# Performance work log

Measured on AMD Instinct MI355X. Metric: run time of the kernel, lower is better.

The kernel has to match this reference:

```python
import jax, jax.numpy as jnp
import numpy as np

N = 50000      # nodes
E = 800000     # edges
IN = 128       # input feature dim
HID = 64       # out_channels per head
HEADS = 2
OUT = 40       # num classes
SLOPE = 0.2    # leaky relu negative slope
EPS = 1e-16    # PyG softmax denominator epsilon


def _xavier(key, shape):
    fan_out, fan_in = shape[0], shape[1]
    a = float(np.sqrt(6.0 / (fan_in + fan_out)))
    return jax.random.uniform(key, shape, minval=-a, maxval=a, dtype=jnp.float32)


def setup_inputs() -> dict:
    key = jax.random.key(0)
    ks = jax.random.split(key, 16)
    x = jax.random.normal(ks[0], (N, IN), dtype=jnp.float32)
    edge_index = jax.random.randint(ks[1], (2, E), 0, N, dtype=jnp.int64)
    # GAT layer 1: lin_l == lin_r (shared), weight [H*C, in], att [C, H]
    W1 = _xavier(ks[2], (HEADS * HID, IN))
    b1 = jnp.zeros((HEADS * HID,), jnp.float32)
    al1 = _xavier(ks[3], (HID, HEADS))
    ar1 = _xavier(ks[4], (HID, HEADS))
    # GAT layer 2: input dim = heads*hidden
    W2 = _xavier(ks[5], (HEADS * HID, HEADS * HID))
    b2 = jnp.zeros((HEADS * HID,), jnp.float32)
    al2 = _xavier(ks[6], (HID, HEADS))
    ar2 = _xavier(ks[7], (HID, HEADS))
    # post_mp: Linear(heads*hid, hid) -> Linear(hid, out)
    Wp1 = _xavier(ks[8], (HID, HEADS * HID))
    bp1 = jnp.zeros((HID,), jnp.float32)
    Wp2 = _xavier(ks[9], (OUT, HID))
    bp2 = jnp.zeros((OUT,), jnp.float32)
    return dict(x=x, edge_index=edge_index, W1=W1, b1=b1, al1=al1, ar1=ar1,
                W2=W2, b2=b2, al2=al2, ar2=ar2, Wp1=Wp1, bp1=bp1, Wp2=Wp2, bp2=bp2)


def gat_layer(x, edge_index, W, b, att_l, att_r):
    """One GAT layer: shared linear, per-edge leaky-relu scores,
    segment-softmax keyed by destination node, scatter-sum."""
    n = x.shape[0]
    xt = (x @ W.T + b).reshape(n, HEADS, HID)          # [N, H, C] (x_l == x_r)
    alpha_l = jnp.einsum('nhc,ch->nh', xt, att_l)      # [N, H]
    alpha_r = jnp.einsum('nhc,ch->nh', xt, att_r)      # [N, H]
    src, dst = edge_index[0], edge_index[1]            # j = source, i = dest
    e = jax.nn.leaky_relu(alpha_r[dst] + alpha_l[src], SLOPE)   # [E, H]
    # segment softmax over edges grouped by destination node
    seg_max = jax.ops.segment_max(e, dst, num_segments=n)       # [N, H]
    ex = jnp.exp(e - seg_max[dst])
    denom = jax.ops.segment_sum(ex, dst, num_segments=n)        # [N, H]
    alpha = ex / (denom[dst] + EPS)                              # [E, H]
    msg = alpha[:, :, None] * xt[src]                            # [E, H, C]
    out = jax.ops.segment_sum(msg, dst, num_segments=n)          # [N, H, C]
    return out.reshape(n, HEADS * HID)


def reference(x, edge_index, W1, b1, al1, ar1, W2, b2, al2, ar2, Wp1, bp1, Wp2, bp2):
    h = jax.nn.relu(gat_layer(x, edge_index, W1, b1, al1, ar1))
    h = jax.nn.relu(gat_layer(h, edge_index, W2, b2, al2, ar2))
    h = h @ Wp1.T + bp1
    h = h @ Wp2.T + bp2
    return jax.nn.log_softmax(h, axis=1)
```

## Files before the change

kernel.cpp:

```cpp
#include <hip/hip_runtime.h>
#include <hip/hip_fp16.h>
#include <cmath>

#define N_NODES 50000
#define N_EDGES 800000
#define F 128
#define OUT_DIM 40
#define SLOPE 0.2f
#define EPS_DEN 1e-16f

#define BK_SHIFT 7
#define BKSZ 128
#define NBK ((N_NODES + BKSZ - 1) / BKSZ)
#define BK_CAP2 2560
#define SC_CHUNK 2500
#define SC_BLOCKS ((N_EDGES + SC_CHUNK - 1) / SC_CHUNK)
#define GEMM_TILES ((N_NODES + 127) / 128)
#define A_BLOCKS (SC_BLOCKS + 25 + GEMM_TILES)
#define SMEM_BYTES 21504
#define POISON ((int)0xAAAAAAAA)

typedef _Float16 half8 __attribute__((ext_vector_type(8)));
typedef float floatx4 __attribute__((ext_vector_type(4)));

struct ScatterS { int sd[SC_CHUNK]; short sb[SC_CHUNK]; int h[NBK]; int lofs[NBK]; };
struct GemmS    { __half Ah[128][40]; __half Bh[128][40]; };
static_assert(sizeof(ScatterS) <= SMEM_BYTES, "scatter LDS");
static_assert(sizeof(GemmS)    <= SMEM_BYTES, "gemm LDS");

__device__ __forceinline__ int swz(int row, int chunk) {
  return row * 128 + ((chunk ^ (row & 15)) << 3);
}

__device__ inline float4 load4(const float* p) { return *(const float4*)p; }
__device__ inline float4 load4(const __half* p) {
  uint2 u = *(const uint2*)p;
  float2 a = __half22float2(*(__half2*)&u.x);
  float2 b = __half22float2(*(__half2*)&u.y);
  return make_float4(a.x, a.y, b.x, b.y);
}

__device__ __forceinline__ void scatter_phase(const int* __restrict__ ei,
    int* __restrict__ bcur, int* __restrict__ pairs, int it, int tid, char* smem_) {
  ScatterS* S = (ScatterS*)smem_;
  for (int i = tid; i < NBK; i += 256) S->h[i] = 0;
  __syncthreads();
  int base = it * SC_CHUNK;
  int end = base + SC_CHUNK; if (end > N_EDGES) end = N_EDGES;
  int cnt = end - base;
  for (int e = base + tid; e < end; e += 256) {
    int s = ei[e];
    int d = ei[N_EDGES + e];
    int b = d >> BK_SHIFT;
    S->sd[e - base] = (s << BK_SHIFT) | (d & (BKSZ - 1));
    S->sb[e - base] = (short)b;
    atomicAdd(&S->h[b], 1);
  }
  __syncthreads();
  for (int i = tid; i < NBK; i += 256)
    if (S->h[i]) {
      S->lofs[i] = i * BK_CAP2 + (atomicAdd(&bcur[i], S->h[i]) - POISON);
      S->h[i] = 0;
    }
  __syncthreads();
  for (int i = tid; i < cnt; i += 256) {
    int b = S->sb[i];
    int pos = S->lofs[b] + atomicAdd(&S->h[b], 1);
    pairs[pos] = S->sd[i];
  }
}

__device__ __forceinline__ void combine_phase(const float* __restrict__ Wp1,
    const float* __restrict__ bp1, const float* __restrict__ Wp2,
    const float* __restrict__ bp2, __half* __restrict__ Wch,
    float* __restrict__ bc, int it, int tid) {
  if (it < 24) {
    int idx = it * 256 + tid;
    int o = idx >> 7, k = idx & 127;
    float s = 0.f;
    if (o < OUT_DIM) {
#pragma unroll 8
      for (int j = 0; j < 64; ++j) s += Wp2[o * 64 + j] * Wp1[j * 128 + k];
    }
    Wch[o * 128 + k] = __float2half(s);
  } else if (tid < 48) {
    int o = tid;
    if (o < OUT_DIM) {
      float s = bp2[o];
      for (int j = 0; j < 64; ++j) s += Wp2[o * 64 + j] * bp1[j];
      bc[o] = s;
    } else {
      bc[o] = -1e30f;
    }
  }
}

__global__ void local_sort_fwd();
template <typename T>
__device__ __forceinline__ void gemm_phase(const T* __restrict__ A,
    const float* __restrict__ W, const float* __restrict__ b,
    const float* __restrict__ attl, const float* __restrict__ attr,
    __half* __restrict__ Ch, float* __restrict__ al, float* __restrict__ ar,
    int nrows, int tile, int tid, char* smem_) {
  GemmS* S = (GemmS*)smem_;
  int lane = tid & 63, wid = tid >> 6;
  int quad = lane >> 4, col = lane & 15;
  int r0 = tile * 128;
  int rowhalf = wid >> 1, colhalf = wid & 1;
  floatx4 acc[4][4] = {};
  for (int kc = 0; kc < 128; kc += 32) {
    for (int i = tid; i < 512; i += 256) {
      int row = i >> 2, seg = i & 3;
      int gr = r0 + row;
      float4 v0, v1;
      if (gr < nrows) {
        const T* p = A + (size_t)gr * 128 + kc + seg * 8;
        v0 = load4(p); v1 = load4(p + 4);
      } else { v0 = make_float4(0.f,0.f,0.f,0.f); v1 = v0; }
      __half2 h0 = __floats2half2_rn(v0.x, v0.y), h1 = __floats2half2_rn(v0.z, v0.w);
      __half2 h2 = __floats2half2_rn(v1.x, v1.y), h3 = __floats2half2_rn(v1.z, v1.w);
      uint4 pk; pk.x = *(unsigned*)&h0; pk.y = *(unsigned*)&h1;
      pk.z = *(unsigned*)&h2; pk.w = *(unsigned*)&h3;
      *(uint4*)&S->Ah[row][seg * 8] = pk;
      const float* q = W + (size_t)row * 128 + kc + seg * 8;
      float4 w0 = *(const float4*)q, w1 = *(const float4*)(q + 4);
      __half2 g0 = __floats2half2_rn(w0.x, w0.y), g1 = __floats2half2_rn(w0.z, w0.w);
      __half2 g2 = __floats2half2_rn(w1.x, w1.y), g3 = __floats2half2_rn(w1.z, w1.w);
      uint4 qk; qk.x = *(unsigned*)&g0; qk.y = *(unsigned*)&g1;
      qk.z = *(unsigned*)&g2; qk.w = *(unsigned*)&g3;
      *(uint4*)&S->Bh[row][seg * 8] = qk;
    }
    __syncthreads();
    half8 afr[4], bfr[4];
#pragma unroll
    for (int rt = 0; rt < 4; ++rt)
      afr[rt] = *(const half8*)&S->Ah[rowhalf * 64 + rt * 16 + col][quad * 8];
#pragma unroll
    for (int ct = 0; ct < 4; ++ct)
      bfr[ct] = *(const half8*)&S->Bh[colhalf * 64 + ct * 16 + col][quad * 8];
#pragma unroll
    for (int rt = 0; rt < 4; ++rt)
#pragma unroll
      for (int ct = 0; ct < 4; ++ct)
        acc[rt][ct] = __builtin_amdgcn_mfma_f32_16x16x32_f16(afr[rt], bfr[ct],
                                                             acc[rt][ct], 0, 0, 0);
    __syncthreads();
  }
  int head = colhalf;
  float bj[4], wl4[4], wr4[4];
#pragma unroll
  for (int ct = 0; ct < 4; ++ct) {
    int c = ct * 16 + col;
    bj[ct] = b[head * 64 + c];
    wl4[ct] = attl[c * 2 + head];
    wr4[ct] = attr[c * 2 + head];
  }
#pragma unroll
  for (int rt = 0; rt < 4; ++rt) {
#pragma unroll
    for (int reg = 0; reg < 4; ++reg) {
      int gr = r0 + rowhalf * 64 + rt * 16 + quad * 4 + reg;
      bool ok = gr < nrows;
      float pl = 0.f, pr = 0.f;
#pragma unroll
      for (int ct = 0; ct < 4; ++ct) {
        float v = acc[rt][ct][reg] + bj[ct];
        pl += v * wl4[ct]; pr += v * wr4[ct];
        if (ok) Ch[(size_t)gr * F + head * 64 + ct * 16 + col] = __float2half(v);
      }
      pl += __shfl_xor(pl, 1, 64); pr += __shfl_xor(pr, 1, 64);
      pl += __shfl_xor(pl, 2, 64); pr += __shfl_xor(pr, 2, 64);
      pl += __shfl_xor(pl, 4, 64); pr += __shfl_xor(pr, 4, 64);
      pl += __shfl_xor(pl, 8, 64); pr += __shfl_xor(pr, 8, 64);
      if (ok && col == 0) { al[gr * 2 + head] = pl; ar[gr * 2 + head] = pr; }
    }
  }
}

__global__ __launch_bounds__(256) void kernelA(const int* __restrict__ ei,
    int* __restrict__ bcur, int* __restrict__ pairs,
    const float* __restrict__ Wp1, const float* __restrict__ bp1,
    const float* __restrict__ Wp2, const float* __restrict__ bp2,
    __half* __restrict__ Wch, float* __restrict__ bc,
    const float* __restrict__ x, const float* __restrict__ W1,
    const float* __restrict__ b1, const float* __restrict__ al1,
    const float* __restrict__ ar1, __half* __restrict__ xh,
    float* __restrict__ al, float* __restrict__ ar) {
  __shared__ __align__(16) char smem[SMEM_BYTES];
  int bid = blockIdx.x, tid = threadIdx.x;
  if (bid < SC_BLOCKS) {
    scatter_phase(ei, bcur, pairs, bid, tid, smem);
  } else if (bid < SC_BLOCKS + 25) {
    combine_phase(Wp1, bp1, Wp2, bp2, Wch, bc, bid - SC_BLOCKS, tid);
  } else {
    gemm_phase<float>(x, W1, b1, al1, ar1, xh, al, ar, N_NODES,
                      bid - SC_BLOCKS - 25, tid, smem);
  }
}

__global__ __launch_bounds__(256) void local_sort(const int* __restrict__ bcur,
    const int* __restrict__ pairs, int* __restrict__ rowstart,
    int* __restrict__ rowend, int* __restrict__ srcs) {
  __shared__ int buf[BK_CAP2];
  __shared__ int sorted[BK_CAP2];
  __shared__ int hist[BKSZ];
  __shared__ int cur[BKSZ];
  int tid = threadIdx.x;
  int b = blockIdx.x;
  int base = b * BK_CAP2;
  int cnt = bcur[b] - POISON;
  if (cnt > BK_CAP2) cnt = BK_CAP2;
  if (cnt < 0) cnt = 0;
  if (tid < BKSZ) hist[tid] = 0;
  __syncthreads();
  for (int i = tid; i < cnt; i += 256) {
    int p = pairs[base + i];
    buf[i] = p;
    atomicAdd(&hist[p & (BKSZ - 1)], 1);
  }
  __syncthreads();
  if (tid < 64) {
    int lane = tid;
    int carry = 0;
#pragma unroll
    for (int c = 0; c < BKSZ; c += 64) {
      int v = hist[c + lane];
      int x = v;
#pragma unroll
      for (int off = 1; off < 64; off <<= 1) {
        int t = __shfl_up(x, off, 64);
        if (lane >= off) x += t;
      }
      int excl = carry + x - v;
      cur[c + lane] = excl;
      int node = b * BKSZ + c + lane;
      if (node < N_NODES) {
        rowstart[node] = base + excl;
        rowend[node]   = base + excl + v;
      }
      carry += __shfl(x, 63, 64);
    }
  }
  __syncthreads();
  for (int i = tid; i < cnt; i += 256) {
    int p = buf[i];
    int pos = atomicAdd(&cur[p & (BKSZ - 1)], 1);
    sorted[pos] = p >> BK_SHIFT;
  }
  __syncthreads();
  for (int i = tid; i < cnt; i += 256)
    srcs[base + i] = sorted[i];
}

__device__ __forceinline__ void agg_node_to_lds(const int* __restrict__ rowstart,
    const int* __restrict__ rowend, const int* __restrict__ srcs,
    const float* __restrict__ al, const float* __restrict__ ar,
    const __half* __restrict__ xsrc, __half* __restrict__ ldsA,
    float (*ebufw)[64], int* sbufw, int node, int ldsrow, int lane) {
  int g = lane >> 4, q = lane & 15;
  int head = q >> 3;
  if (node >= N_NODES) {
    if (g == 0) {
      uint4 z = {0, 0, 0, 0};
      *(uint4*)&ldsA[swz(ldsrow, q)] = z;
    }
    __builtin_amdgcn_wave_barrier();
    return;
  }
  int start = rowstart[node], end = rowend[node];
  float2 arv = *(const float2*)(ar + (size_t)node * 2);
  float ar0 = arv.x, ar1 = arv.y;
  const float* wrow = &ebufw[head][0];
  const __half* xbase = xsrc + q * 8;
  float acc[8] = {};
  float dl0 = 0.f, dl1 = 0.f;
  for (int c = start; c < end; c += 64) {
    int j = c + lane;
    float e0 = 0.f, e1 = 0.f; int soff = 0;
    if (j < end) {
      int s = srcs[j];
      soff = s << BK_SHIFT;
      float2 a = *(const float2*)(al + (size_t)s * 2);
      float s0 = a.x + ar0; s0 = (s0 > 0.f) ? s0 : SLOPE * s0;
      float s1 = a.y + ar1; s1 = (s1 > 0.f) ? s1 : SLOPE * s1;
      e0 = __expf(s0); e1 = __expf(s1);
    }
    dl0 += e0; dl1 += e1;
    ebufw[0][lane] = e0; ebufw[1][lane] = e1; sbufw[lane] = soff;
    __builtin_amdgcn_wave_barrier();
    int cend = end - c; if (cend > 64) cend = 64;
#pragma unroll 4
    for (int t = 0; t < cend; t += 4) {
      int te = t + g;
      if (te < cend) {
        int so = sbufw[te];
        float w = wrow[te];
        uint4 u = *(const uint4*)(xbase + so);
        const __half2* hh = (const __half2*)&u;
        float2 f0 = __half22float2(hh[0]);
        float2 f1 = __half22float2(hh[1]);
        float2 f2 = __half22float2(hh[2]);
        float2 f3 = __half22float2(hh[3]);
        acc[0] += w * f0.x; acc[1] += w * f0.y;
        acc[2] += w * f1.x; acc[3] += w * f1.y;
        acc[4] += w * f2.x; acc[5] += w * f2.y;
        acc[6] += w * f3.x; acc[7] += w * f3.y;
      }
    }
    __builtin_amdgcn_wave_barrier();
  }
#pragma unroll
  for (int off = 32; off > 0; off >>= 1) {
    dl0 += __shfl_xor(dl0, off, 64);
    dl1 += __shfl_xor(dl1, off, 64);
  }
#pragma unroll
  for (int k = 0; k < 8; ++k) {
    acc[k] += __shfl_xor(acc[k], 16, 64);
    acc[k] += __shfl_xor(acc[k], 32, 64);
  }
  if (g == 0) {
    float d = (head == 0) ? dl0 : dl1;
    float inv = 1.f / (d + EPS_DEN);
    __half2 o0 = __floats2half2_rn(fmaxf(acc[0] * inv, 0.f), fmaxf(acc[1] * inv, 0.f));
    __half2 o1 = __floats2half2_rn(fmaxf(acc[2] * inv, 0.f), fmaxf(acc[3] * inv, 0.f));
    __half2 o2 = __floats2half2_rn(fmaxf(acc[4] * inv, 0.f), fmaxf(acc[5] * inv, 0.f));
    __half2 o3 = __floats2half2_rn(fmaxf(acc[6] * inv, 0.f), fmaxf(acc[7] * inv, 0.f));
    uint4 pack;
    pack.x = *(unsigned*)&o0; pack.y = *(unsigned*)&o1;
    pack.z = *(unsigned*)&o2; pack.w = *(unsigned*)&o3;
    *(uint4*)&ldsA[swz(ldsrow, q)] = pack;
  }
  __builtin_amdgcn_wave_barrier();
}

__global__ __launch_bounds__(1024) void fusedB(const int* __restrict__ rowstart,
    const int* __restrict__ rowend, const int* __restrict__ srcs,
    const float* __restrict__ al, const float* __restrict__ ar,
    const __half* __restrict__ xh,
    const float* __restrict__ W2, const float* __restrict__ b2,
    const float* __restrict__ attl, const float* __restrict__ attr,
    __half* __restrict__ xh2, float* __restrict__ al2, float* __restrict__ ar2) {
  __shared__ __half Ah[128 * 128];
  __shared__ __half Bh[128 * 128];
  __shared__ float ebuf[16][2][64];
  __shared__ int   sbuf[16][64];
  int tid = threadIdx.x;
  int wid = tid >> 6, lane = tid & 63;
  int tile = blockIdx.x;
#pragma unroll
  for (int r = 0; r < 2; ++r) {
    int j = tid + r * 1024;
    int row = j >> 4, c = j & 15;
    const float* q = W2 + (size_t)row * 128 + c * 8;
    float4 w0 = *(const float4*)q, w1 = *(const float4*)(q + 4);
    __half2 g0 = __floats2half2_rn(w0.x, w0.y), g1 = __floats2half2_rn(w0.z, w0.w);
    __half2 g2 = __floats2half2_rn(w1.x, w1.y), g3 = __floats2half2_rn(w1.z, w1.w);
    uint4 qk; qk.x = *(unsigned*)&g0; qk.y = *(unsigned*)&g1;
    qk.z = *(unsigned*)&g2; qk.w = *(unsigned*)&g3;
    *(uint4*)&Bh[swz(row, c)] = qk;
  }
#pragma unroll 1
  for (int r = 0; r < 8; ++r) {
    int ldsrow = r * 16 + wid;
    agg_node_to_lds(rowstart, rowend, srcs, al, ar, xh, Ah,
                    ebuf[wid], sbuf[wid], tile * 128 + ldsrow, ldsrow, lane);
  }
  __syncthreads();
  int rowg = wid >> 1, colg = wid & 1;
  int quad = lane >> 4, col = lane & 15;
  floatx4 acc[4] = {};
#pragma unroll
  for (int kc4 = 0; kc4 < 4; ++kc4) {
    int arow = rowg * 16 + col;
    half8 afr = *(const half8*)&Ah[swz(arow, (kc4 << 2) | quad)];
#pragma unroll
    for (int ct = 0; ct < 4; ++ct) {
      int brow = colg * 64 + ct * 16 + col;
      half8 bfr = *(const half8*)&Bh[swz(brow, (kc4 << 2) | quad)];
      acc[ct] = __builtin_amdgcn_mfma_f32_16x16x32_f16(afr, bfr, acc[ct], 0, 0, 0);
    }
  }
  int head = colg;
  float bj[4], wl4[4], wr4[4];
#pragma unroll
  for (int ct = 0; ct < 4; ++ct) {
    int c = ct * 16 + col;
    bj[ct] = b2[head * 64 + c];
    wl4[ct] = attl[c * 2 + head];
    wr4[ct] = attr[c * 2 + head];
  }
#pragma unroll
  for (int reg = 0; reg < 4; ++reg) {
    int gr = tile * 128 + rowg * 16 + quad * 4 + reg;
    bool ok = gr < N_NODES;
    float pl = 0.f, pr = 0.f;
#pragma unroll
    for (int ct = 0; ct < 4; ++ct) {
      float v = acc[ct][reg] + bj[ct];
      pl += v * wl4[ct]; pr += v * wr4[ct];
      if (ok) xh2[(size_t)gr * F + head * 64 + ct * 16 + col] = __float2half(v);
    }
    pl += __shfl_xor(pl, 1, 64); pr += __shfl_xor(pr, 1, 64);
    pl += __shfl_xor(pl, 2, 64); pr += __shfl_xor(pr, 2, 64);
    pl += __shfl_xor(pl, 4, 64); pr += __shfl_xor(pr, 4, 64);
    pl += __shfl_xor(pl, 8, 64); pr += __shfl_xor(pr, 8, 64);
    if (ok && col == 0) { al2[gr * 2 + head] = pl; ar2[gr * 2 + head] = pr; }
  }
}

__global__ __launch_bounds__(1024) void fusedC(const int* __restrict__ rowstart,
    const int* __restrict__ rowend, const int* __restrict__ srcs,
    const float* __restrict__ al2, const float* __restrict__ ar2,
    const __half* __restrict__ xh2,
    const __half* __restrict__ Wch, const float* __restrict__ bc,
    float* __restrict__ out) {
  __shared__ __half Ah[128 * 128];
  __shared__ float ebuf[16][2][64];
  __shared__ int   sbuf[16][64];
  int tid = threadIdx.x;
  int wid = tid >> 6, lane = tid & 63;
  int tile = blockIdx.x;
#pragma unroll 1
  for (int r = 0; r < 8; ++r) {
    int ldsrow = r * 16 + wid;
    agg_node_to_lds(rowstart, rowend, srcs, al2, ar2, xh2, Ah,
                    ebuf[wid], sbuf[wid], tile * 128 + ldsrow, ldsrow, lane);
  }
  __syncthreads();
  if (wid >= 8) return;
  int quad = lane >> 4, col = lane & 15;
  int rbase = wid * 16;
  floatx4 acc[3] = {};
#pragma unroll
  for (int kc4 = 0; kc4 < 4; ++kc4) {
    half8 afr = *(const half8*)&Ah[swz(rbase + col, (kc4 << 2) | quad)];
#pragma unroll
    for (int ct = 0; ct < 3; ++ct) {
      half8 bfr = *(const half8*)(Wch + (size_t)(ct * 16 + col) * 128 + kc4 * 32 + quad * 8);
      acc[ct] = __builtin_amdgcn_mfma_f32_16x16x32_f16(afr, bfr, acc[ct], 0, 0, 0);
    }
  }
  float bcv[3];
#pragma unroll
  for (int ct = 0; ct < 3; ++ct) bcv[ct] = bc[ct * 16 + col];
#pragma unroll
  for (int reg = 0; reg < 4; ++reg) {
    int row = tile * 128 + rbase + quad * 4 + reg;
    float z[3], m = -INFINITY;
#pragma unroll
    for (int ct = 0; ct < 3; ++ct) { z[ct] = acc[ct][reg] + bcv[ct]; m = fmaxf(m, z[ct]); }
    m = fmaxf(m, __shfl_xor(m, 1, 64));
    m = fmaxf(m, __shfl_xor(m, 2, 64));
    m = fmaxf(m, __shfl_xor(m, 4, 64));
    m = fmaxf(m, __shfl_xor(m, 8, 64));
    float s = 0.f;
#pragma unroll
    for (int ct = 0; ct < 3; ++ct) s += __expf(z[ct] - m);
    s += __shfl_xor(s, 1, 64);
    s += __shfl_xor(s, 2, 64);
    s += __shfl_xor(s, 4, 64);
    s += __shfl_xor(s, 8, 64);
    float ls = logf(s);
    if (row < N_NODES) {
#pragma unroll
      for (int ct = 0; ct < 3; ++ct) {
        int o = ct * 16 + col;
        if (o < OUT_DIM) out[(size_t)row * OUT_DIM + o] = z[ct] - m - ls;
      }
    }
  }
}

extern "C" void kernel_launch(void* const* d_in, const int* in_sizes, int n_in,
                              void* d_out, int out_size, void* d_ws, size_t ws_size,
                              hipStream_t stream) {
  const float* x   = (const float*)d_in[0];
  const int*   ei  = (const int*)d_in[1];
  const float* W1  = (const float*)d_in[2];
  const float* b1  = (const float*)d_in[3];
  const float* al1 = (const float*)d_in[4];
  const float* ar1 = (const float*)d_in[5];
  const float* W2  = (const float*)d_in[6];
  const float* b2  = (const float*)d_in[7];
  const float* al2w= (const float*)d_in[8];
  const float* ar2w= (const float*)d_in[9];
  const float* Wp1 = (const float*)d_in[10];
  const float* bp1 = (const float*)d_in[11];
  const float* Wp2 = (const float*)d_in[12];
  const float* bp2 = (const float*)d_in[13];
  float* out = (float*)d_out;

  float* al    = (float*)d_ws;
  float* ar    = al + (size_t)N_NODES * 2;
  float* al2   = ar + (size_t)N_NODES * 2;
  float* ar2   = al2 + (size_t)N_NODES * 2;
  __half* Wch  = (__half*)(ar2 + (size_t)N_NODES * 2);
  float* bc    = (float*)(Wch + 48 * 128);
  int* rowstart= (int*)(bc + 48);
  int* rowend  = rowstart + N_NODES;
  int* bcur    = rowend + N_NODES;
  int* srcs    = bcur + NBK;
  int* pairs   = srcs + NBK * BK_CAP2;
  uintptr_t pp = ((uintptr_t)(pairs + NBK * BK_CAP2) + 255) & ~(uintptr_t)255;
  __half* xh   = (__half*)pp;
  __half* xh2  = xh + (size_t)N_NODES * F;

  kernelA<<<A_BLOCKS, 256, 0, stream>>>(ei, bcur, pairs, Wp1, bp1, Wp2, bp2,
                                        Wch, bc, x, W1, b1, al1, ar1, xh, al, ar);
  local_sort<<<NBK, 256, 0, stream>>>(bcur, pairs, rowstart, rowend, srcs);
  fusedB<<<GEMM_TILES, 1024, 0, stream>>>(rowstart, rowend, srcs, al, ar, xh,
                                          W2, b2, al2w, ar2w, xh2, al2, ar2);
  fusedC<<<GEMM_TILES, 1024, 0, stream>>>(rowstart, rowend, srcs, al2, ar2, xh2,
                                          Wch, bc, out);
}
```

Measured before the change: 218.0 us.

## Shrink aggregation tiles to 32 rows and precompute fp16 W2 once

After: 256.5 us. 1.18x slower.

```diff
diff --git a/kernel.cpp b/kernel.cpp
--- a/kernel.cpp
+++ b/kernel.cpp
@@ -16,9 +16,13 @@
 #define SC_CHUNK 2500
 #define SC_BLOCKS ((N_EDGES + SC_CHUNK - 1) / SC_CHUNK)
 #define GEMM_TILES ((N_NODES + 127) / 128)
-#define A_BLOCKS (SC_BLOCKS + 25 + GEMM_TILES)
+#define CB_BLOCKS 33
+#define A_BLOCKS (SC_BLOCKS + CB_BLOCKS + GEMM_TILES)
 #define SMEM_BYTES 21504
 #define POISON ((int)0xAAAAAAAA)
+
+#define AGG_TILE 32
+#define AGG_TILES ((N_NODES + AGG_TILE - 1) / AGG_TILE)
 
 typedef _Float16 half8 __attribute__((ext_vector_type(8)));
 typedef float floatx4 __attribute__((ext_vector_type(4)));
@@ -72,8 +76,9 @@
 
 __device__ __forceinline__ void combine_phase(const float* __restrict__ Wp1,
     const float* __restrict__ bp1, const float* __restrict__ Wp2,
-    const float* __restrict__ bp2, __half* __restrict__ Wch,
-    float* __restrict__ bc, int it, int tid) {
+    const float* __restrict__ bp2, const float* __restrict__ W2,
+    __half* __restrict__ Wch, float* __restrict__ bc,
+    __half* __restrict__ W2h, int it, int tid) {
   if (it < 24) {
     int idx = it * 256 + tid;
     int o = idx >> 7, k = idx & 127;
@@ -83,19 +88,29 @@
       for (int j = 0; j < 64; ++j) s += Wp2[o * 64 + j] * Wp1[j * 128 + k];
     }
     Wch[o * 128 + k] = __float2half(s);
-  } else if (tid < 48) {
-    int o = tid;
-    if (o < OUT_DIM) {
-      float s = bp2[o];
-      for (int j = 0; j < 64; ++j) s += Wp2[o * 64 + j] * bp1[j];
-      bc[o] = s;
-    } else {
-      bc[o] = -1e30f;
-    }
-  }
-}
-
-__global__ void local_sort_fwd();
+  } else if (it == 24) {
+    if (tid < 48) {
+      int o = tid;
+      if (o < OUT_DIM) {
+        float s = bp2[o];
+        for (int j = 0; j < 64; ++j) s += Wp2[o * 64 + j] * bp1[j];
+        bc[o] = s;
+      } else {
+        bc[o] = -1e30f;
+      }
+    }
+  } else {
+    int idx = (it - 25) * 2048 + tid * 8;
+    const float* q = W2 + idx;
+    float4 w0 = *(const float4*)q, w1 = *(const float4*)(q + 4);
+    __half2 g0 = __floats2half2_rn(w0.x, w0.y), g1 = __floats2half2_rn(w0.z, w0.w);
+    __half2 g2 = __floats2half2_rn(w1.x, w1.y), g3 = __floats2half2_rn(w1.z, w1.w);
+    uint4 qk; qk.x = *(unsigned*)&g0; qk.y = *(unsigned*)&g1;
+    qk.z = *(unsigned*)&g2; qk.w = *(unsigned*)&g3;
+    *(uint4*)&W2h[idx] = qk;
+  }
+}
+
 template <typename T>
 __device__ __forceinline__ void gemm_phase(const T* __restrict__ A,
     const float* __restrict__ W, const float* __restrict__ b,
@@ -181,7 +196,8 @@
     int* __restrict__ bcur, int* __restrict__ pairs,
     const float* __restrict__ Wp1, const float* __restrict__ bp1,
     const float* __restrict__ Wp2, const float* __restrict__ bp2,
-    __half* __restrict__ Wch, float* __restrict__ bc,
+    const float* __restrict__ W2, __half* __restrict__ Wch,
+    float* __restrict__ bc, __half* __restrict__ W2h,
     const float* __restrict__ x, const float* __restrict__ W1,
     const float* __restrict__ b1, const float* __restrict__ al1,
     const float* __restrict__ ar1, __half* __restrict__ xh,
@@ -190,15 +206,15 @@
   int bid = blockIdx.x, tid = threadIdx.x;
   if (bid < SC_BLOCKS) {
     scatter_phase(ei, bcur, pairs, bid, tid, smem);
-  } else if (bid < SC_BLOCKS + 25) {
-    combine_phase(Wp1, bp1, Wp2, bp2, Wch, bc, bid - SC_BLOCKS, tid);
+  } else if (bid < SC_BLOCKS + CB_BLOCKS) {
+    combine_phase(Wp1, bp1, Wp2, bp2, W2, Wch, bc, W2h, bid - SC_BLOCKS, tid);
   } else {
     gemm_phase<float>(x, W1, b1, al1, ar1, xh, al, ar, N_NODES,
-                      bid - SC_BLOCKS - 25, tid, smem);
-  }
-}
-
-__global__ __launch_bounds__(256) void local_sort(const int* __restrict__ bcur,
+                      bid - SC_BLOCKS - CB_BLOCKS, tid, smem);
+  }
+}
+
+__global__ __launch_bounds__(512) void local_sort(const int* __restrict__ bcur,
     const int* __restrict__ pairs, int* __restrict__ rowstart,
     int* __restrict__ rowend, int* __restrict__ srcs) {
   __shared__ int buf[BK_CAP2];
@@ -213,7 +229,7 @@
   if (cnt < 0) cnt = 0;
   if (tid < BKSZ) hist[tid] = 0;
   __syncthreads();
-  for (int i = tid; i < cnt; i += 256) {
+  for (int i = tid; i < cnt; i += 512) {
     int p = pairs[base + i];
     buf[i] = p;
     atomicAdd(&hist[p & (BKSZ - 1)], 1);
@@ -242,13 +258,13 @@
     }
   }
   __syncthreads();
-  for (int i = tid; i < cnt; i += 256) {
+  for (int i = tid; i < cnt; i += 512) {
     int p = buf[i];
     int pos = atomicAdd(&cur[p & (BKSZ - 1)], 1);
     sorted[pos] = p >> BK_SHIFT;
   }
   __syncthreads();
-  for (int i = tid; i < cnt; i += 256)
+  for (int i = tid; i < cnt; i += 512)
     srcs[base + i] = sorted[i];
 }
 
@@ -334,37 +350,24 @@
   __builtin_amdgcn_wave_barrier();
 }
 
-__global__ __launch_bounds__(1024) void fusedB(const int* __restrict__ rowstart,
+__global__ __launch_bounds__(256) void fusedB(const int* __restrict__ rowstart,
     const int* __restrict__ rowend, const int* __restrict__ srcs,
     const float* __restrict__ al, const float* __restrict__ ar,
-    const __half* __restrict__ xh,
-    const float* __restrict__ W2, const float* __restrict__ b2,
+    const __half* __restrict__ xh, const __half* __restrict__ W2h,
+    const float* __restrict__ b2,
     const float* __restrict__ attl, const float* __restrict__ attr,
     __half* __restrict__ xh2, float* __restrict__ al2, float* __restrict__ ar2) {
-  __shared__ __half Ah[128 * 128];
-  __shared__ __half Bh[128 * 128];
-  __shared__ float ebuf[16][2][64];
-  __shared__ int   sbuf[16][64];
+  __shared__ __half Ah[AGG_TILE * 128];
+  __shared__ float ebuf[4][2][64];
+  __shared__ int   sbuf[4][64];
   int tid = threadIdx.x;
   int wid = tid >> 6, lane = tid & 63;
   int tile = blockIdx.x;
-#pragma unroll
-  for (int r = 0; r < 2; ++r) {
-    int j = tid + r * 1024;
-    int row = j >> 4, c = j & 15;
-    const float* q = W2 + (size_t)row * 128 + c * 8;
-    float4 w0 = *(const float4*)q, w1 = *(const float4*)(q + 4);
-    __half2 g0 = __floats2half2_rn(w0.x, w0.y), g1 = __floats2half2_rn(w0.z, w0.w);
-    __half2 g2 = __floats2half2_rn(w1.x, w1.y), g3 = __floats2half2_rn(w1.z, w1.w);
-    uint4 qk; qk.x = *(unsigned*)&g0; qk.y = *(unsigned*)&g1;
-    qk.z = *(unsigned*)&g2; qk.w = *(unsigned*)&g3;
-    *(uint4*)&Bh[swz(row, c)] = qk;
-  }
 #pragma unroll 1
   for (int r = 0; r < 8; ++r) {
-    int ldsrow = r * 16 + wid;
+    int ldsrow = r * 4 + wid;
     agg_node_to_lds(rowstart, rowend, srcs, al, ar, xh, Ah,
-                    ebuf[wid], sbuf[wid], tile * 128 + ldsrow, ldsrow, lane);
+                    ebuf[wid], sbuf[wid], tile * AGG_TILE + ldsrow, ldsrow, lane);
   }
   __syncthreads();
   int rowg = wid >> 1, colg = wid & 1;
@@ -372,12 +375,11 @@
   floatx4 acc[4] = {};
 #pragma unroll
   for (int kc4 = 0; kc4 < 4; ++kc4) {
-    int arow = rowg * 16 + col;
-    half8 afr = *(const half8*)&Ah[swz(arow, (kc4 << 2) | quad)];
+    half8 afr = *(const half8*)&Ah[swz(rowg * 16 + col, (kc4 << 2) | quad)];
 #pragma unroll
     for (int ct = 0; ct < 4; ++ct) {
       int brow = colg * 64 + ct * 16 + col;
-      half8 bfr = *(const half8*)&Bh[swz(brow, (kc4 << 2) | quad)];
+      half8 bfr = *(const half8*)(W2h + (size_t)brow * 128 + kc4 * 32 + quad * 8);
       acc[ct] = __builtin_amdgcn_mfma_f32_16x16x32_f16(afr, bfr, acc[ct], 0, 0, 0);
     }
   }
@@ -392,7 +394,7 @@
   }
 #pragma unroll
   for (int reg = 0; reg < 4; ++reg) {
-    int gr = tile * 128 + rowg * 16 + quad * 4 + reg;
+    int gr = tile * AGG_TILE + rowg * 16 + quad * 4 + reg;
     bool ok = gr < N_NODES;
     float pl = 0.f, pr = 0.f;
 #pragma unroll
@@ -409,26 +411,26 @@
   }
 }
 
-__global__ __launch_bounds__(1024) void fusedC(const int* __restrict__ rowstart,
+__global__ __launch_bounds__(256) void fusedC(const int* __restrict__ rowstart,
     const int* __restrict__ rowend, const int* __restrict__ srcs,
     const float* __restrict__ al2, const float* __restrict__ ar2,
     const __half* __restrict__ xh2,
     const __half* __restrict__ Wch, const float* __restrict__ bc,
     float* __restrict__ out) {
-  __shared__ __half Ah[128 * 128];
-  __shared__ float ebuf[16][2][64];
-  __shared__ int   sbuf[16][64];
+  __shared__ __half Ah[AGG_TILE * 128];
+  __shared__ float ebuf[4][2][64];
+  __shared__ int   sbuf[4][64];
   int tid = threadIdx.x;
   int wid = tid >> 6, lane = tid & 63;
   int tile = blockIdx.x;
 #pragma unroll 1
   for (int r = 0; r < 8; ++r) {
-    int ldsrow = r * 16 + wid;
+    int ldsrow = r * 4 + wid;
     agg_node_to_lds(rowstart, rowend, srcs, al2, ar2, xh2, Ah,
-                    ebuf[wid], sbuf[wid], tile * 128 + ldsrow, ldsrow, lane);
-  }
-  __syncthreads();
-  if (wid >= 8) return;
+                    ebuf[wid], sbuf[wid], tile * AGG_TILE + ldsrow, ldsrow, lane);
+  }
+  __syncthreads();
+  if (wid >= 2) return;
   int quad = lane >> 4, col = lane & 15;
   int rbase = wid * 16;
   floatx4 acc[3] = {};
@@ -446,7 +448,7 @@
   for (int ct = 0; ct < 3; ++ct) bcv[ct] = bc[ct * 16 + col];
 #pragma unroll
   for (int reg = 0; reg < 4; ++reg) {
-    int row = tile * 128 + rbase + quad * 4 + reg;
+    int row = tile * AGG_TILE + rbase + quad * 4 + reg;
     float z[3], m = -INFINITY;
 #pragma unroll
     for (int ct = 0; ct < 3; ++ct) { z[ct] = acc[ct][reg] + bcv[ct]; m = fmaxf(m, z[ct]); }
@@ -497,7 +499,8 @@
   float* ar2   = al2 + (size_t)N_NODES * 2;
   __half* Wch  = (__half*)(ar2 + (size_t)N_NODES * 2);
   float* bc    = (float*)(Wch + 48 * 128);
-  int* rowstart= (int*)(bc + 48);
+  __half* W2h  = (__half*)(bc + 48);
+  int* rowstart= (int*)(W2h + 128 * 128);
   int* rowend  = rowstart + N_NODES;
   int* bcur    = rowend + N_NODES;
   int* srcs    = bcur + NBK;
@@ -507,10 +510,11 @@
   __half* xh2  = xh + (size_t)N_NODES * F;
 
   kernelA<<<A_BLOCKS, 256, 0, stream>>>(ei, bcur, pairs, Wp1, bp1, Wp2, bp2,
-                                        Wch, bc, x, W1, b1, al1, ar1, xh, al, ar);
-  local_sort<<<NBK, 256, 0, stream>>>(bcur, pairs, rowstart, rowend, srcs);
-  fusedB<<<GEMM_TILES, 1024, 0, stream>>>(rowstart, rowend, srcs, al, ar, xh,
-                                          W2, b2, al2w, ar2w, xh2, al2, ar2);
-  fusedC<<<GEMM_TILES, 1024, 0, stream>>>(rowstart, rowend, srcs, al2, ar2, xh2,
-                                          Wch, bc, out);
-}
+                                        W2, Wch, bc, W2h, x, W1, b1, al1, ar1,
+                                        xh, al, ar);
+  local_sort<<<NBK, 512, 0, stream>>>(bcur, pairs, rowstart, rowend, srcs);
+  fusedB<<<AGG_TILES, 256, 0, stream>>>(rowstart, rowend, srcs, al, ar, xh,
+                                        W2h, b2, al2w, ar2w, xh2, al2, ar2);
+  fusedC<<<AGG_TILES, 256, 0, stream>>>(rowstart, rowend, srcs, al2, ar2, xh2,
+                                        Wch, bc, out);
+}
```
